# Optimization experiments

Hardware: AMD Instinct MI355X
Metric: run time of the kernel (lower is better)

The kernel has to match this reference:

```python
import jax, jax.numpy as jnp
import numpy as np
import math

B, L, D, H = 4, 1024, 768, 12   # docs, seq_len, hidden, attn heads
E, M, P = 24, 4, 552            # entities/doc, mentions/entity, pairs/doc
EMB, BLK, NL = 768, 64, 97      # emb_size, block_size, num relation labels


def setup_inputs() -> dict:
    key = jax.random.key(0)
    ks = jax.random.split(key, 12)
    s = 0.02  # weight init scale
    return {
        "sequence_output": jax.random.normal(ks[0], (B, L, D), jnp.float32),
        "attention": jax.random.uniform(ks[1], (B, H, L, L), jnp.float32),
        "W_q": jax.random.normal(ks[2], (D, D), jnp.float32) * s,
        "W_k": jax.random.normal(ks[3], (D, D), jnp.float32) * s,
        "head_W": jax.random.normal(ks[4], (2 * D, EMB), jnp.float32) * s,
        "head_b": jax.random.normal(ks[5], (EMB,), jnp.float32) * s,
        "tail_W": jax.random.normal(ks[6], (2 * D, EMB), jnp.float32) * s,
        "tail_b": jax.random.normal(ks[7], (EMB,), jnp.float32) * s,
        "bil_W": jax.random.normal(ks[8], (EMB * BLK, NL), jnp.float32) * s,
        "bil_b": jax.random.normal(ks[9], (NL,), jnp.float32) * s,
        "mention_pos": jax.random.randint(ks[10], (B, E, M), 0, L - 2),
        "hts": jax.random.randint(ks[11], (B, P, 2), 0, E),
    }


def reference(sequence_output, attention, W_q, W_k, head_W, head_b,
              tail_W, tail_b, bil_W, bil_b, mention_pos, hts):
    offset = 1  # bert-style [CLS] offset
    pos = mention_pos + offset                     # [B,E,M] token index of each mention
    bb = jnp.arange(B)[:, None, None]

    # --- mention gathers (padded version of the ragged python loops) ---
    # per-mention attention rows: attention[b, :, pos, :] -> [B,E,M,H,L]
    att_q = attention.transpose(0, 2, 1, 3)        # [B,L,H,L]
    ment_att = att_q[bb, pos]                      # [B,E,M,H,L]
    ent_att = ment_att.mean(axis=2)                # [B,E,H,L]  (mean over mentions)
    # mention embeddings (GAT stage = identity here): [B,E,M,D]
    ment_emb = sequence_output[bb, pos]

    # --- localized context rs via head*tail attention product ---
    bb2 = jnp.arange(B)[:, None]
    h_att = ent_att[bb2, hts[:, :, 0]]             # [B,P,H,L]
    t_att = ent_att[bb2, hts[:, :, 1]]             # [B,P,H,L]
    ht_att = (h_att * t_att).mean(axis=2)          # [B,P,L] (mean over heads)
    ht_att = ht_att / (ht_att.sum(axis=-1, keepdims=True) + 1e-5)
    rs = jnp.einsum('bld,bpl->bpd', sequence_output, ht_att)  # [B,P,D]

    R = B * P
    rs_f = rs.reshape(R, D)

    # --- entity representations via mention-level attention pooling ---
    h_ment = ment_emb[bb2, hts[:, :, 0]].reshape(R, M, D)
    t_ment = ment_emb[bb2, hts[:, :, 1]].reshape(R, M, D)
    q_c = rs_f @ W_q                               # [R,D]
    inv = 1.0 / math.sqrt(D)

    def pool(ment):
        k = ment.reshape(-1, D) @ W_k
        k = k.reshape(R, M, D)
        scores = jnp.einsum('rmd,rd->rm', k, q_c) * inv
        w = jax.nn.softmax(scores, axis=-1)
        return jnp.einsum('rm,rmd->rd', w, ment)

    h_ent = pool(h_ment)                           # [R,D]
    t_ent = pool(t_ment)                           # [R,D]

    # --- extractors + grouped bilinear classifier ---
    hs = jnp.tanh(jnp.concatenate([h_ent, rs_f], axis=1) @ head_W + head_b)
    ts = jnp.tanh(jnp.concatenate([t_ent, rs_f], axis=1) @ tail_W + tail_b)
    K = EMB // BLK
    b1 = hs.reshape(R, K, BLK)
    b2 = ts.reshape(R, K, BLK)
    bl = (b1[:, :, :, None] * b2[:, :, None, :]).reshape(R, EMB * BLK)
    logits = bl @ bil_W + bil_b                    # [R,NL]
    return logits
```

## Files before the change

kernel.cpp:

```cpp
#include <hip/hip_runtime.h>
#include <hip/hip_bf16.h>
#include <math.h>

#define Bc 4
#define Lc 1024
#define Dc 768
#define Hc 12
#define Ec 24
#define Mc 4
#define Pc 552
#define EMBc 768
#define NLc 97
#define Rc (Bc*Pc)
#define KSPL 48
#define HT_ABS (35*32*512)

typedef __attribute__((ext_vector_type(4))) float f32x4;
typedef __attribute__((ext_vector_type(8))) short short8;
typedef __attribute__((ext_vector_type(4))) unsigned short us4;
typedef _Float16 f16x8 __attribute__((ext_vector_type(8)));

static __device__ __forceinline__ unsigned short f2bf(float x){
  unsigned int u = __float_as_uint(x);
  unsigned int r = u + 0x7fffu + ((u >> 16) & 1u);
  return (unsigned short)(r >> 16);
}
static __device__ __forceinline__ unsigned short f2h(float x){
  _Float16 h = (_Float16)x;
  return __builtin_bit_cast(unsigned short, h);
}
static __device__ __forceinline__ float h2f(unsigned short x){
  return (float)__builtin_bit_cast(_Float16, x);
}
static __device__ __forceinline__ size_t flin_off(int r, int kk, int KT){
  return ((size_t)(r>>4)*KT + (kk>>5))*512 + (size_t)((((kk&31)>>3)*16 + (r&15))*8) + (kk&7);
}

__global__ __launch_bounds__(256) void k_prep(const float* __restrict__ bilW, unsigned short* __restrict__ Wbf,
                                              const float* __restrict__ seq, unsigned short* __restrict__ seqf,
                                              const float* __restrict__ W_q, unsigned short* __restrict__ Wq_f,
                                              const float* __restrict__ W_k, unsigned short* __restrict__ Wk_f,
                                              const float* __restrict__ headW, unsigned short* __restrict__ headW_f,
                                              const float* __restrict__ tailW, unsigned short* __restrict__ tailW_f,
                                              const float* __restrict__ att, const int* __restrict__ mpos,
                                              float* __restrict__ ent_att,
                                              float* __restrict__ ment, unsigned short* __restrict__ ment_bf){
  int bx = blockIdx.x;
  int tid = threadIdx.x;
  __shared__ float t[64][65];
  if (bx < 1536){
    const float* Ws = bilW + (size_t)bx*32*NLc;
    unsigned short* o = Wbf + (size_t)bx*4480;
    float* w = &t[0][0];
    for (int idx = tid; idx < 32*NLc; idx += 256)
      w[idx] = Ws[idx];
    __syncthreads();
    #pragma unroll
    for (int q8 = 0; q8 < 18; q8++){
      int idx = q8*256 + tid;
      if (idx < 4480){
        int n = idx / 40, kk = idx - n*40;
        float v = (kk < 32 && n < NLc) ? w[kk*NLc + n] : 0.f;
        o[idx] = f2h(v);
      }
    }
    return;
  }
  if (bx >= 3168){
    int blk = bx - 3168;
    int h  = blk % Hc;
    int be = blk / Hc;
    int b  = be / Ec;
    int p0 = mpos[be*Mc+0]+1, p1 = mpos[be*Mc+1]+1;
    int p2 = mpos[be*Mc+2]+1, p3 = mpos[be*Mc+3]+1;
    const float* ab = att + ((size_t)b*Hc + h)*Lc*Lc;
    const float* a0 = ab + (size_t)p0*Lc;
    const float* a1 = ab + (size_t)p1*Lc;
    const float* a2 = ab + (size_t)p2*Lc;
    const float* a3 = ab + (size_t)p3*Lc;
    float* o = ent_att + (size_t)blk*Lc;
    int l4 = tid*4;
    float4 v0 = *(const float4*)(a0 + l4);
    float4 v1 = *(const float4*)(a1 + l4);
    float4 v2 = *(const float4*)(a2 + l4);
    float4 v3 = *(const float4*)(a3 + l4);
    float4 ov;
    ov.x = 0.25f*(v0.x+v1.x+v2.x+v3.x);
    ov.y = 0.25f*(v0.y+v1.y+v2.y+v3.y);
    ov.z = 0.25f*(v0.z+v1.z+v2.z+v3.z);
    ov.w = 0.25f*(v0.w+v1.w+v2.w+v3.w);
    *(float4*)(o + l4) = ov;
    int gidx = blk*256 + tid;
    int d = gidx % Dc;
    int bem = gidx / Dc;
    int bb = bem / (Ec*Mc);
    int pos = mpos[bem] + 1;
    float v = seq[((size_t)bb*Lc + pos)*Dc + d];
    ment[gidx] = v;
    ment_bf[flin_off(bem, d, 24)] = f2bf(v);
    return;
  }
  bx -= 1536;
  const float* src; unsigned short* dst; int tk, tn, KTW;
  if (bx < 768){
    int z = bx / 192, rem = bx % 192;
    src = seq + (size_t)z*Lc*Dc; dst = seqf + (size_t)z*(Dc/16)*(Lc/32)*512;
    tk = rem % 16; tn = rem / 16; KTW = 32;
  } else if (bx < 768+144){
    int rem = bx - 768;
    src = W_q; dst = Wq_f; tk = rem % 12; tn = rem / 12; KTW = 24;
  } else if (bx < 768+288){
    int rem = bx - (768+144);
    src = W_k; dst = Wk_f; tk = rem % 12; tn = rem / 12; KTW = 24;
  } else if (bx < 768+288+288){
    int rem = bx - (768+288);
    src = headW; dst = headW_f; tk = rem % 24; tn = rem / 24; KTW = 48;
  } else {
    int rem = bx - (768+288+288);
    src = tailW; dst = tailW_f; tk = rem % 24; tn = rem / 24; KTW = 48;
  }
  int r0 = tk*64, c0 = tn*64;
  #pragma unroll
  for (int q8 = 0; q8 < 16; q8++){
    int idx = q8*256 + tid;
    int rr = idx >> 6, cc = idx & 63;
    t[rr][cc] = src[(size_t)(r0+rr)*768 + c0+cc];
  }
  __syncthreads();
  #pragma unroll
  for (int q8 = 0; q8 < 16; q8++){
    int idx = q8*256 + tid;
    int li = idx & 511, sub = idx >> 9;
    int nt_l = sub >> 1, kt_l = sub & 1;
    int lane = li >> 3, e = li & 7;
    int kl = kt_l*32 + (lane>>4)*8 + e;
    int nl = nt_l*16 + (lane&15);
    dst[ ((size_t)(c0/16 + nt_l)*KTW + (r0/32 + kt_l))*512 + li ] = f2bf(t[kl][nl]);
  }
}

__global__ __launch_bounds__(256) void k_ht_att(const float* __restrict__ ent_att,
                                                const int* __restrict__ hts,
                                                unsigned short* __restrict__ htbf){
  int b = blockIdx.x & 3;
  int p = blockIdx.x >> 2;
  unsigned short* o = htbf + (size_t)b*HT_ABS;
  int l4 = threadIdx.x*4;
  if (p >= Pc){
    us4 z4 = {0,0,0,0};
    *(us4*)(o + flin_off(p, l4, 32)) = z4;
    return;
  }
  int r = b*Pc + p;
  int hi = hts[r*2+0], ti = hts[r*2+1];
  const float* eh = ent_att + (size_t)(b*Ec+hi)*Hc*Lc;
  const float* et = ent_att + (size_t)(b*Ec+ti)*Hc*Lc;
  __shared__ float raw[Lc];
  __shared__ float wsum[4];
  float4 s4 = {0.f,0.f,0.f,0.f};
  #pragma unroll
  for (int h = 0; h < Hc; h++){
    float4 e1 = *(const float4*)&eh[h*Lc + l4];
    float4 e2 = *(const float4*)&et[h*Lc + l4];
    s4.x = fmaf(e1.x,e2.x,s4.x); s4.y = fmaf(e1.y,e2.y,s4.y);
    s4.z = fmaf(e1.z,e2.z,s4.z); s4.w = fmaf(e1.w,e2.w,s4.w);
  }
  s4.x *= (1.0f/Hc); s4.y *= (1.0f/Hc); s4.z *= (1.0f/Hc); s4.w *= (1.0f/Hc);
  *(float4*)&raw[l4] = s4;
  float lsum = s4.x+s4.y+s4.z+s4.w;
  for (int off = 32; off; off >>= 1) lsum += __shfl_down(lsum, off);
  if ((threadIdx.x & 63) == 0) wsum[threadIdx.x>>6] = lsum;
  __syncthreads();
  float inv = 1.0f/(wsum[0]+wsum[1]+wsum[2]+wsum[3] + 1e-5f);
  float4 rv = *(const float4*)&raw[l4];
  us4 v4;
  v4[0] = f2bf(rv.x*inv); v4[1] = f2bf(rv.y*inv);
  v4[2] = f2bf(rv.z*inv); v4[3] = f2bf(rv.w*inv);
  *(us4*)(o + flin_off(p, l4, 32)) = v4;
}

struct FJob {
  const unsigned short* A1; const unsigned short* A2;
  const unsigned short* W;  const float* bias; void* C;
  int M; int mtmax; size_t Abs; size_t Wbs; int rowsPerBatch;
};

template<int KT1, int KT2, int CT, int NT>
__global__ __launch_bounds__(256) void k_fgemm(FJob j0, FJob j1, int nx0){
  FJob j = (blockIdx.x < nx0) ? j0 : j1;
  int mbx = (blockIdx.x < nx0) ? blockIdx.x : blockIdx.x - nx0;
  const int KTW = KT1 + KT2;
  int z = blockIdx.z;
  int lane = threadIdx.x & 63, wid = threadIdx.x >> 6;
  int row16 = lane & 15, oct = lane >> 4;
  int rb = mbx*128 + wid*32;
  int mt0 = rb >> 4;       if (mt0 >= j.mtmax) mt0 = j.mtmax - 1;
  int mt1 = (rb >> 4) + 1; if (mt1 >= j.mtmax) mt1 = j.mtmax - 1;
  const unsigned short* ap0 = j.A1 + (size_t)z*j.Abs + (size_t)mt0*KT1*512 + lane*8;
  const unsigned short* ap1 = j.A1 + (size_t)z*j.Abs + (size_t)mt1*KT1*512 + lane*8;
  const unsigned short* wb = j.W  + (size_t)z*j.Wbs + (size_t)(blockIdx.y*NT)*KTW*512 + lane*8;
  f32x4 acc[2][NT];
  #pragma unroll
  for (int m = 0; m < 2; m++)
    #pragma unroll
    for (int n = 0; n < NT; n++) acc[m][n] = (f32x4){0.f,0.f,0.f,0.f};
  #pragma unroll 4
  for (int kt = 0; kt < KT1; kt++){
    short8 a0 = *(const short8*)(ap0 + (size_t)kt*512);
    short8 a1 = *(const short8*)(ap1 + (size_t)kt*512);
    #pragma unroll
    for (int n = 0; n < NT; n++){
      short8 bv = *(const short8*)(wb + (size_t)(n*KTW + kt)*512);
      acc[0][n] = __builtin_amdgcn_mfma_f32_16x16x32_bf16(a0, bv, acc[0][n], 0, 0, 0);
      acc[1][n] = __builtin_amdgcn_mfma_f32_16x16x32_bf16(a1, bv, acc[1][n], 0, 0, 0);
    }
  }
  if (KT2 > 0){
    const unsigned short* b0p = j.A2 + (size_t)mt0*KT2*512 + lane*8;
    const unsigned short* b1p = j.A2 + (size_t)mt1*KT2*512 + lane*8;
    #pragma unroll 4
    for (int kt = 0; kt < KT2; kt++){
      short8 a0 = *(const short8*)(b0p + (size_t)kt*512);
      short8 a1 = *(const short8*)(b1p + (size_t)kt*512);
      #pragma unroll
      for (int n = 0; n < NT; n++){
        short8 bv = *(const short8*)(wb + (size_t)(n*KTW + KT1 + kt)*512);
        acc[0][n] = __builtin_amdgcn_mfma_f32_16x16x32_bf16(a0, bv, acc[0][n], 0, 0, 0);
        acc[1][n] = __builtin_amdgcn_mfma_f32_16x16x32_bf16(a1, bv, acc[1][n], 0, 0, 0);
      }
    }
  }
  int colb = blockIdx.y*(NT*16);
  #pragma unroll
  for (int m = 0; m < 2; m++)
    #pragma unroll
    for (int n = 0; n < NT; n++)
      #pragma unroll
      for (int jj = 0; jj < 4; jj++){
        int r = rb + m*16 + oct*4 + jj;
        if (r < j.M){
          int col = colb + n*16 + row16;
          float v = acc[m][n][jj];
          if (CT <= 1 && j.bias) v += j.bias[col];
          int rg = z*j.rowsPerBatch + r;
          if (CT == 2){
            ((unsigned short*)j.C)[flin_off(rg, col, 24)] = f2bf(v);
          } else if (CT == 1){
            ((unsigned short*)j.C)[(size_t)rg*768 + col] = f2h(tanhf(v));
          } else {
            ((float*)j.C)[(size_t)rg*768 + col] = v;
          }
        }
      }
}

__global__ __launch_bounds__(256) void k_pool(const float* __restrict__ kment,
                                              const float* __restrict__ ment,
                                              const float* __restrict__ q_c,
                                              const int* __restrict__ hts,
                                              unsigned short* __restrict__ h_bf,
                                              unsigned short* __restrict__ t_bf){
  int wid = threadIdx.x >> 6, lane = threadIdx.x & 63;
  int r = blockIdx.x*4 + wid;
  int b = r / Pc;
  float q[12];
  const float* qp = q_c + (size_t)r*Dc + lane;
  #pragma unroll
  for (int u = 0; u < 12; u++) q[u] = qp[u*64];
  const float invs = 0.03608439182435161f;
  #pragma unroll
  for (int side = 0; side < 2; side++){
    int e = hts[r*2+side];
    const float* kb = kment + (size_t)(b*Ec+e)*Mc*Dc + lane;
    const float* mb = ment  + (size_t)(b*Ec+e)*Mc*Dc;
    float part[Mc] = {0.f,0.f,0.f,0.f};
    #pragma unroll
    for (int m = 0; m < Mc; m++)
      #pragma unroll
      for (int u = 0; u < 12; u++)
        part[m] = fmaf(kb[m*Dc + u*64], q[u], part[m]);
    #pragma unroll
    for (int m = 0; m < Mc; m++)
      #pragma unroll
      for (int off = 1; off < 64; off <<= 1)
        part[m] += __shfl_xor(part[m], off);
    float mx = fmaxf(fmaxf(part[0],part[1]), fmaxf(part[2],part[3])) * invs;
    float w0 = expf(part[0]*invs - mx), w1 = expf(part[1]*invs - mx);
    float w2 = expf(part[2]*invs - mx), w3 = expf(part[3]*invs - mx);
    float isum = 1.0f/(w0+w1+w2+w3);
    w0 *= isum; w1 *= isum; w2 *= isum; w3 *= isum;
    unsigned short* o = side ? t_bf : h_bf;
    #pragma unroll
    for (int u = 0; u < 12; u++){
      int d = lane + u*64;
      float v = w0*mb[d] + w1*mb[Dc+d] + w2*mb[2*Dc+d] + w3*mb[3*Dc+d];
      o[flin_off(r, d, 24)] = f2bf(v);
    }
  }
}

__global__ __launch_bounds__(256) void k_bilinear_mfma(
    const unsigned short* __restrict__ hs16, const unsigned short* __restrict__ ts16,
    const unsigned short* __restrict__ Wbf,
    unsigned short* __restrict__ partial)
{
  int mb = blockIdx.x / KSPL;
  int kb = blockIdx.x % KSPL;
  int k  = kb >> 2;
  int i0 = (kb & 3) * 16;

  int tid  = threadIdx.x;
  int lane = tid & 63;
  int wid  = tid >> 6;
  int row16 = lane & 15;
  int oct   = lane >> 4;

  int rbase = mb*256 + wid*64;

  __shared__ __align__(16) unsigned short Wlds[2][8960];

  f16x8 tsh[4][2];
  f16x8 hsh[4][2];
  #pragma unroll
  for (int m = 0; m < 4; m++){
    int r = rbase + m*16 + row16; if (r > Rc-1) r = Rc-1;
    const unsigned short* tp = ts16 + (size_t)r*EMBc + k*64;
    tsh[m][0] = __builtin_bit_cast(f16x8, *(const short8*)(tp + oct*8));
    tsh[m][1] = __builtin_bit_cast(f16x8, *(const short8*)(tp + 32 + oct*8));
    const unsigned short* hp = hs16 + (size_t)r*EMBc + k*64 + i0;
    hsh[m][0] = __builtin_bit_cast(f16x8, *(const short8*)(hp));
    hsh[m][1] = __builtin_bit_cast(f16x8, *(const short8*)(hp + 8));
  }

  const char* wsrc = (const char*)(Wbf + ((size_t)(k*128 + i0*2))*4480);

  #pragma unroll
  for (int rr = 0; rr < 5; rr++){
    int u = tid + rr*256;
    if (u < 1120)
      __builtin_amdgcn_global_load_lds(
        (const __attribute__((address_space(1))) unsigned int*)(wsrc + (size_t)u*16),
        (__attribute__((address_space(3))) unsigned int*)((char*)&Wlds[0][0] + u*16),
        16, 0, 0);
  }

  f32x4 acc[4][7];
  #pragma unroll
  for (int m = 0; m < 4; m++)
    #pragma unroll
    for (int n = 0; n < 7; n++) acc[m][n] = (f32x4){0.f,0.f,0.f,0.f};

  __syncthreads();

  #pragma unroll
  for (int cp = 0; cp < 16; cp++){
    int cur = cp & 1;
    if (cp < 15){
      const char* nsrc = wsrc + (size_t)(cp+1)*17920;
      #pragma unroll
      for (int rr = 0; rr < 5; rr++){
        int u = tid + rr*256;
        if (u < 1120)
          __builtin_amdgcn_global_load_lds(
            (const __attribute__((address_space(1))) unsigned int*)(nsrc + (size_t)u*16),
            (__attribute__((address_space(3))) unsigned int*)((char*)&Wlds[cur^1][0] + u*16),
            16, 0, 0);
      }
    }
    #pragma unroll
    for (int half = 0; half < 2; half++){
      f16x8 af[4];
      #pragma unroll
      for (int m = 0; m < 4; m++){
        _Float16 hv = hsh[m][cp>>3][cp&7];
        f16x8 hvb = {hv,hv,hv,hv,hv,hv,hv,hv};
        af[m] = tsh[m][half] * hvb;
      }
      #pragma unroll
      for (int n = 0; n < 7; n++){
        f16x8 bfr = __builtin_bit_cast(f16x8,
            *(const short8*)&Wlds[cur][half*4480 + (n*16 + row16)*40 + oct*8]);
        #pragma unroll
        for (int m = 0; m < 4; m++)
          acc[m][n] = __builtin_amdgcn_mfma_f32_16x16x32_f16(af[m], bfr, acc[m][n], 0, 0, 0);
      }
    }
    __syncthreads();
  }

  unsigned short* pk = partial + (size_t)kb*Rc*NLc;
  #pragma unroll
  for (int m = 0; m < 4; m++){
    #pragma unroll
    for (int n = 0; n < 7; n++){
      #pragma unroll
      for (int j = 0; j < 4; j++){
        int r = rbase + m*16 + oct*4 + j;
        int col = n*16 + row16;
        if (r < Rc && col < NLc)
          pk[(size_t)r*NLc + col] = f2h(acc[m][n][j]);
      }
    }
  }
}

__global__ __launch_bounds__(256) void k_reduce(const unsigned short* __restrict__ partial,
                                                const float* __restrict__ bilb,
                                                float* __restrict__ out){
  int idx = blockIdx.x*256 + threadIdx.x;
  if (idx >= Rc*NLc) return;
  int n = idx % NLc;
  float s = bilb[n];
  #pragma unroll
  for (int ks = 0; ks < KSPL; ks++) s += h2f(partial[(size_t)ks*Rc*NLc + idx]);
  out[idx] = s;
}

extern "C" void kernel_launch(void* const* d_in, const int* in_sizes, int n_in,
                              void* d_out, int out_size, void* d_ws, size_t ws_size,
                              hipStream_t stream){
  const float* seq   = (const float*)d_in[0];
  const float* att   = (const float*)d_in[1];
  const float* W_q   = (const float*)d_in[2];
  const float* W_k   = (const float*)d_in[3];
  const float* headW = (const float*)d_in[4];
  const float* headb = (const float*)d_in[5];
  const float* tailW = (const float*)d_in[6];
  const float* tailb = (const float*)d_in[7];
  const float* bilW  = (const float*)d_in[8];
  const float* bilb  = (const float*)d_in[9];
  const int*   mpos  = (const int*)d_in[10];
  const int*   hts   = (const int*)d_in[11];
  float* out = (float*)d_out;

  float* ws = (float*)d_ws;
  float* ent_att = ws;
  float* q_c     = ws + 1179648;
  float* kment   = q_c + 1695744;
  float* ment    = kment + 294912;
  unsigned short* seqf    = (unsigned short*)(ment + 294912);
  unsigned short* htbf    = seqf + 3145728;
  unsigned short* rs_bf   = htbf + 4*HT_ABS;
  unsigned short* ment_bf = rs_bf + 1695744;
  unsigned short* h_bf    = ment_bf + 294912;
  unsigned short* t_bf    = h_bf + 1695744;
  unsigned short* Wq_f    = t_bf + 1695744;
  unsigned short* Wk_f    = Wq_f + 589824;
  unsigned short* headW_f = Wk_f + 589824;
  unsigned short* tailW_f = headW_f + 1179648;
  unsigned short* hs16 = tailW_f + 1179648;
  unsigned short* ts16 = hs16 + 1695744;
  unsigned short* Wbf  = ts16 + 1695744;
  unsigned short* partial = (unsigned short*)ws;

  k_prep   <<<4320, 256, 0, stream>>>(bilW, Wbf, seq, seqf, W_q, Wq_f, W_k, Wk_f,
                                      headW, headW_f, tailW, tailW_f,
                                      att, mpos, ent_att, ment, ment_bf);
  k_ht_att <<<4*560, 256, 0, stream>>>(ent_att, hts, htbf);
  {
    FJob jrs = { htbf, nullptr, seqf, nullptr, rs_bf, Pc, 35,
                 (size_t)HT_ABS, (size_t)(48*32*512), Pc };
    k_fgemm<32,0,2,2><<<dim3(5,24,4), 256, 0, stream>>>(jrs, jrs, 5);
  }
  {
    FJob jq = { rs_bf,   nullptr, Wq_f, nullptr, q_c,   Rc,       138, 0, 0, 0 };
    FJob jk = { ment_bf, nullptr, Wk_f, nullptr, kment, Bc*Ec*Mc,  24, 0, 0, 0 };
    k_fgemm<24,0,0,2><<<dim3(21,24), 256, 0, stream>>>(jq, jk, 18);
  }
  k_pool   <<<Rc/4, 256, 0, stream>>>(kment, ment, q_c, hts, h_bf, t_bf);
  {
    FJob jh = { h_bf, rs_bf, headW_f, headb, hs16, Rc, 138, 0, 0, 0 };
    FJob jt = { t_bf, rs_bf, tailW_f, tailb, ts16, Rc, 138, 0, 0, 0 };
    k_fgemm<24,24,1,2><<<dim3(36,24), 256, 0, stream>>>(jh, jt, 18);
  }
  k_bilinear_mfma<<<9*KSPL, 256, 0, stream>>>(hs16, ts16, Wbf, partial);
  k_reduce <<<(Rc*NLc+255)/256, 256, 0, stream>>>(partial, bilb, out);
}
```

Before: 146.6 us.

## Precompute mention and context projections to fold pooling into extractor GEMM

Uses linearity: h_ent@W_h equals the softmax-weighted sum of (mention@W_h), so the mention embeddings (384 rows) and rs are projected once through the head and tail weights. k_pool then combines the precomputed projections, adds bias and applies tanh. The separate extractor GEMM over 2208 rows with K=1536 is replaced by rs and mention projection jobs batched into one multi-job launch with the q/k GEMMs. In exchange it writes more fp32 intermediates (rsWh, rsWt) and adds a gather-heavy pool step, and the extractor now sums fp32 projections of bf16-rounded mentions instead of projecting a bf16-rounded pooled vector.

```diff
diff --git a/kernel.cpp b/kernel.cpp
--- a/kernel.cpp
+++ b/kernel.cpp
@@ -44,7 +44,7 @@
                                               const float* __restrict__ tailW, unsigned short* __restrict__ tailW_f,
                                               const float* __restrict__ att, const int* __restrict__ mpos,
                                               float* __restrict__ ent_att,
-                                              float* __restrict__ ment, unsigned short* __restrict__ ment_bf){
+                                              unsigned short* __restrict__ ment_bf){
   int bx = blockIdx.x;
   int tid = threadIdx.x;
   __shared__ float t[64][65];
@@ -96,7 +96,6 @@
     int bb = bem / (Ec*Mc);
     int pos = mpos[bem] + 1;
     float v = seq[((size_t)bb*Lc + pos)*Dc + d];
-    ment[gidx] = v;
     ment_bf[flin_off(bem, d, 24)] = f2bf(v);
     return;
   }
@@ -180,16 +179,21 @@
 }
 
 struct FJob {
-  const unsigned short* A1; const unsigned short* A2;
-  const unsigned short* W;  const float* bias; void* C;
-  int M; int mtmax; size_t Abs; size_t Wbs; int rowsPerBatch;
+  const unsigned short* A1; const unsigned short* W; const float* bias; void* C;
+  int M; int mtmax; int Wktw; int rowsPerBatch;
+  size_t Abs; size_t Wbs;
 };
-
-template<int KT1, int KT2, int CT, int NT>
-__global__ __launch_bounds__(256) void k_fgemm(FJob j0, FJob j1, int nx0){
-  FJob j = (blockIdx.x < nx0) ? j0 : j1;
-  int mbx = (blockIdx.x < nx0) ? blockIdx.x : blockIdx.x - nx0;
-  const int KTW = KT1 + KT2;
+struct FJobs {
+  FJob j[6]; int xs[7]; int n;
+};
+
+template<int KT1, int CT, int NT>
+__global__ __launch_bounds__(256) void k_fgemmN(FJobs P){
+  int jx = 0;
+  for (int tjob = 1; tjob < P.n; tjob++)
+    if ((int)blockIdx.x >= P.xs[tjob]) jx = tjob;
+  FJob j = P.j[jx];
+  int mbx = blockIdx.x - P.xs[jx];
   int z = blockIdx.z;
   int lane = threadIdx.x & 63, wid = threadIdx.x >> 6;
   int row16 = lane & 15, oct = lane >> 4;
@@ -198,7 +202,7 @@
   int mt1 = (rb >> 4) + 1; if (mt1 >= j.mtmax) mt1 = j.mtmax - 1;
   const unsigned short* ap0 = j.A1 + (size_t)z*j.Abs + (size_t)mt0*KT1*512 + lane*8;
   const unsigned short* ap1 = j.A1 + (size_t)z*j.Abs + (size_t)mt1*KT1*512 + lane*8;
-  const unsigned short* wb = j.W  + (size_t)z*j.Wbs + (size_t)(blockIdx.y*NT)*KTW*512 + lane*8;
+  const unsigned short* wb = j.W + (size_t)z*j.Wbs + (size_t)(blockIdx.y*NT)*j.Wktw*512 + lane*8;
   f32x4 acc[2][NT];
   #pragma unroll
   for (int m = 0; m < 2; m++)
@@ -210,24 +214,9 @@
     short8 a1 = *(const short8*)(ap1 + (size_t)kt*512);
     #pragma unroll
     for (int n = 0; n < NT; n++){
-      short8 bv = *(const short8*)(wb + (size_t)(n*KTW + kt)*512);
+      short8 bv = *(const short8*)(wb + (size_t)(n*j.Wktw + kt)*512);
       acc[0][n] = __builtin_amdgcn_mfma_f32_16x16x32_bf16(a0, bv, acc[0][n], 0, 0, 0);
       acc[1][n] = __builtin_amdgcn_mfma_f32_16x16x32_bf16(a1, bv, acc[1][n], 0, 0, 0);
-    }
-  }
-  if (KT2 > 0){
-    const unsigned short* b0p = j.A2 + (size_t)mt0*KT2*512 + lane*8;
-    const unsigned short* b1p = j.A2 + (size_t)mt1*KT2*512 + lane*8;
-    #pragma unroll 4
-    for (int kt = 0; kt < KT2; kt++){
-      short8 a0 = *(const short8*)(b0p + (size_t)kt*512);
-      short8 a1 = *(const short8*)(b1p + (size_t)kt*512);
-      #pragma unroll
-      for (int n = 0; n < NT; n++){
-        short8 bv = *(const short8*)(wb + (size_t)(n*KTW + KT1 + kt)*512);
-        acc[0][n] = __builtin_amdgcn_mfma_f32_16x16x32_bf16(a0, bv, acc[0][n], 0, 0, 0);
-        acc[1][n] = __builtin_amdgcn_mfma_f32_16x16x32_bf16(a1, bv, acc[1][n], 0, 0, 0);
-      }
     }
   }
   int colb = blockIdx.y*(NT*16);
@@ -241,12 +230,10 @@
         if (r < j.M){
           int col = colb + n*16 + row16;
           float v = acc[m][n][jj];
-          if (CT <= 1 && j.bias) v += j.bias[col];
+          if (CT == 0 && j.bias) v += j.bias[col];
           int rg = z*j.rowsPerBatch + r;
           if (CT == 2){
             ((unsigned short*)j.C)[flin_off(rg, col, 24)] = f2bf(v);
-          } else if (CT == 1){
-            ((unsigned short*)j.C)[(size_t)rg*768 + col] = f2h(tanhf(v));
           } else {
             ((float*)j.C)[(size_t)rg*768 + col] = v;
           }
@@ -255,11 +242,16 @@
 }
 
 __global__ __launch_bounds__(256) void k_pool(const float* __restrict__ kment,
-                                              const float* __restrict__ ment,
                                               const float* __restrict__ q_c,
+                                              const float* __restrict__ rsWh,
+                                              const float* __restrict__ rsWt,
+                                              const float* __restrict__ mWh,
+                                              const float* __restrict__ mWt,
+                                              const float* __restrict__ headb,
+                                              const float* __restrict__ tailb,
                                               const int* __restrict__ hts,
-                                              unsigned short* __restrict__ h_bf,
-                                              unsigned short* __restrict__ t_bf){
+                                              unsigned short* __restrict__ hs16,
+                                              unsigned short* __restrict__ ts16){
   int wid = threadIdx.x >> 6, lane = threadIdx.x & 63;
   int r = blockIdx.x*4 + wid;
   int b = r / Pc;
@@ -272,7 +264,6 @@
   for (int side = 0; side < 2; side++){
     int e = hts[r*2+side];
     const float* kb = kment + (size_t)(b*Ec+e)*Mc*Dc + lane;
-    const float* mb = ment  + (size_t)(b*Ec+e)*Mc*Dc;
     float part[Mc] = {0.f,0.f,0.f,0.f};
     #pragma unroll
     for (int m = 0; m < Mc; m++)
@@ -289,12 +280,16 @@
     float w2 = expf(part[2]*invs - mx), w3 = expf(part[3]*invs - mx);
     float isum = 1.0f/(w0+w1+w2+w3);
     w0 *= isum; w1 *= isum; w2 *= isum; w3 *= isum;
-    unsigned short* o = side ? t_bf : h_bf;
+    const float* mW  = (side ? mWt  : mWh) + (size_t)(b*Ec+e)*Mc*Dc;
+    const float* rsW = (side ? rsWt : rsWh) + (size_t)r*Dc;
+    const float* bias = side ? tailb : headb;
+    unsigned short* o = (side ? ts16 : hs16) + (size_t)r*Dc;
     #pragma unroll
     for (int u = 0; u < 12; u++){
       int d = lane + u*64;
-      float v = w0*mb[d] + w1*mb[Dc+d] + w2*mb[2*Dc+d] + w3*mb[3*Dc+d];
-      o[flin_off(r, d, 24)] = f2bf(v);
+      float v = rsW[d] + bias[d]
+              + w0*mW[d] + w1*mW[Dc+d] + w2*mW[2*Dc+d] + w3*mW[3*Dc+d];
+      o[d] = f2h(tanhf(v));
     }
   }
 }
@@ -437,42 +432,49 @@
   float* ent_att = ws;
   float* q_c     = ws + 1179648;
   float* kment   = q_c + 1695744;
-  float* ment    = kment + 294912;
-  unsigned short* seqf    = (unsigned short*)(ment + 294912);
+  float* ment_unused = kment + 294912;
+  unsigned short* seqf    = (unsigned short*)(ment_unused + 294912);
   unsigned short* htbf    = seqf + 3145728;
   unsigned short* rs_bf   = htbf + 4*HT_ABS;
   unsigned short* ment_bf = rs_bf + 1695744;
-  unsigned short* h_bf    = ment_bf + 294912;
-  unsigned short* t_bf    = h_bf + 1695744;
-  unsigned short* Wq_f    = t_bf + 1695744;
+  unsigned short* Wq_f    = ment_bf + 294912;
   unsigned short* Wk_f    = Wq_f + 589824;
   unsigned short* headW_f = Wk_f + 589824;
   unsigned short* tailW_f = headW_f + 1179648;
   unsigned short* hs16 = tailW_f + 1179648;
   unsigned short* ts16 = hs16 + 1695744;
   unsigned short* Wbf  = ts16 + 1695744;
+  float* rsWh = (float*)(Wbf + 6881280);
+  float* rsWt = rsWh + 1695744;
+  float* mWh  = rsWt + 1695744;
+  float* mWt  = mWh + 294912;
   unsigned short* partial = (unsigned short*)ws;
 
   k_prep   <<<4320, 256, 0, stream>>>(bilW, Wbf, seq, seqf, W_q, Wq_f, W_k, Wk_f,
                                       headW, headW_f, tailW, tailW_f,
-                                      att, mpos, ent_att, ment, ment_bf);
+                                      att, mpos, ent_att, ment_bf);
   k_ht_att <<<4*560, 256, 0, stream>>>(ent_att, hts, htbf);
   {
-    FJob jrs = { htbf, nullptr, seqf, nullptr, rs_bf, Pc, 35,
-                 (size_t)HT_ABS, (size_t)(48*32*512), Pc };
-    k_fgemm<32,0,2,2><<<dim3(5,24,4), 256, 0, stream>>>(jrs, jrs, 5);
+    FJobs P{};
+    P.j[0] = { htbf, seqf, nullptr, rs_bf, Pc, 35, 32, Pc,
+               (size_t)HT_ABS, (size_t)(48*32*512) };
+    P.xs[0] = 0; P.xs[1] = 5; P.n = 1;
+    k_fgemmN<32,2,2><<<dim3(5,24,4), 256, 0, stream>>>(P);
   }
   {
-    FJob jq = { rs_bf,   nullptr, Wq_f, nullptr, q_c,   Rc,       138, 0, 0, 0 };
-    FJob jk = { ment_bf, nullptr, Wk_f, nullptr, kment, Bc*Ec*Mc,  24, 0, 0, 0 };
-    k_fgemm<24,0,0,2><<<dim3(21,24), 256, 0, stream>>>(jq, jk, 18);
-  }
-  k_pool   <<<Rc/4, 256, 0, stream>>>(kment, ment, q_c, hts, h_bf, t_bf);
-  {
-    FJob jh = { h_bf, rs_bf, headW_f, headb, hs16, Rc, 138, 0, 0, 0 };
-    FJob jt = { t_bf, rs_bf, tailW_f, tailb, ts16, Rc, 138, 0, 0, 0 };
-    k_fgemm<24,24,1,2><<<dim3(36,24), 256, 0, stream>>>(jh, jt, 18);
-  }
+    FJobs P{};
+    P.j[0] = { rs_bf,   Wq_f,              nullptr, q_c,   Rc,  138, 24, 0, 0, 0 };
+    P.j[1] = { ment_bf, Wk_f,              nullptr, kment, 384,  24, 24, 0, 0, 0 };
+    P.j[2] = { rs_bf,   headW_f + 24*512,  nullptr, rsWh,  Rc,  138, 48, 0, 0, 0 };
+    P.j[3] = { rs_bf,   tailW_f + 24*512,  nullptr, rsWt,  Rc,  138, 48, 0, 0, 0 };
+    P.j[4] = { ment_bf, headW_f,           nullptr, mWh,   384,  24, 48, 0, 0, 0 };
+    P.j[5] = { ment_bf, tailW_f,           nullptr, mWt,   384,  24, 48, 0, 0, 0 };
+    P.xs[0]=0; P.xs[1]=18; P.xs[2]=21; P.xs[3]=39; P.xs[4]=57; P.xs[5]=60; P.xs[6]=63;
+    P.n = 6;
+    k_fgemmN<24,0,2><<<dim3(63,24), 256, 0, stream>>>(P);
+  }
+  k_pool   <<<Rc/4, 256, 0, stream>>>(kment, q_c, rsWh, rsWt, mWh, mWt,
+                                      headb, tailb, hts, hs16, ts16);
   k_bilinear_mfma<<<9*KSPL, 256, 0, stream>>>(hs16, ts16, Wbf, partial);
   k_reduce <<<(Rc*NLc+255)/256, 256, 0, stream>>>(partial, bilb, out);
 }
```

New measurement: 134.1 us. 1.09x faster.
